# Kernel tuning notes

Measured on AMD Instinct MI355X. Metric: run time of the kernel, lower is better.

Reference implementation:

```python
import jax, jax.numpy as jnp
import numpy as np

N_NODES = 50000
N_EDGES = 600000
N_GRAPHS = 64
D_IN = 128
D_HID = 128
D_OUT = 64


def setup_inputs() -> dict:
    key = jax.random.key(0)
    ks = jax.random.split(key, 8)
    x = jax.random.normal(ks[0], (N_NODES, D_IN), dtype=jnp.float32)
    edge_index = jax.random.randint(ks[1], (2, N_EDGES), 0, N_NODES, dtype=jnp.int64)
    batch = jnp.sort(jax.random.randint(ks[2], (N_NODES,), 0, N_GRAPHS, dtype=jnp.int64))
    def glorot(k, fan_in, fan_out):
        s = jnp.sqrt(6.0 / (fan_in + fan_out))
        return jax.random.uniform(k, (fan_in, fan_out), jnp.float32, -s, s)
    return {
        "x": x, "edge_index": edge_index, "batch": batch,
        "W1": glorot(ks[3], D_IN, D_HID), "b1": jnp.zeros((D_HID,), jnp.float32),
        "W2": glorot(ks[4], D_HID, D_HID), "b2": jnp.zeros((D_HID,), jnp.float32),
        "W3": glorot(ks[5], D_HID, D_HID), "b3": jnp.zeros((D_HID,), jnp.float32),
        "W4": glorot(ks[6], D_HID, D_OUT), "b4": jnp.zeros((D_OUT,), jnp.float32),
    }


def _gcn_conv(x, W, b, src, dst, deg_inv_sqrt, n_nodes):
    # PyG GCNConv: h = x W; out_i = sum_{j->i} norm_ij h_j  (+ self loop) + b
    h = x @ W  # [N, F]
    norm = deg_inv_sqrt[src] * deg_inv_sqrt[dst]  # [E]
    agg = jax.ops.segment_sum(h[src] * norm[:, None], dst, num_segments=n_nodes)
    # self-loop contribution: norm_ii = deg_inv_sqrt[i]^2
    agg = agg + h * (deg_inv_sqrt * deg_inv_sqrt)[:, None]
    return agg + b


def reference(x, edge_index, batch, W1, b1, W2, b2, W3, b3, W4, b4):
    n = x.shape[0]
    src, dst = edge_index[0], edge_index[1]
    # degree including self loops (PyG add_self_loops + deg over dst)
    deg = jax.ops.segment_sum(jnp.ones_like(dst, dtype=x.dtype), dst, num_segments=n) + 1.0
    deg_inv_sqrt = jax.lax.rsqrt(deg)

    h = jax.nn.relu(_gcn_conv(x, W1, b1, src, dst, deg_inv_sqrt, n))
    h = jax.nn.relu(_gcn_conv(h, W2, b2, src, dst, deg_inv_sqrt, n))
    h = jax.nn.relu(_gcn_conv(h, W3, b3, src, dst, deg_inv_sqrt, n))
    h = _gcn_conv(h, W4, b4, src, dst, deg_inv_sqrt, n)

    # global mean pool over graphs in the batch
    sums = jax.ops.segment_sum(h, batch, num_segments=N_GRAPHS)  # [G, D_OUT]
    cnts = jax.ops.segment_sum(jnp.ones((n,), h.dtype), batch, num_segments=N_GRAPHS)
    hg = sums / jnp.maximum(cnts, 1.0)[:, None]
    return jnp.squeeze(hg)
```

## Files before the change

### kernel.cpp

```cpp
#include <hip/hip_runtime.h>
#include <hip/hip_bf16.h>
#include <hip/hip_fp16.h>

#define N_NODES 50000
#define N_EDGES 600000
#define N_GRAPHS 64
#define PCHUNK 16

typedef __attribute__((ext_vector_type(8))) short bf16x8;
typedef __attribute__((ext_vector_type(4))) float f32x4;

__device__ __forceinline__ unsigned short f2bf(float f) {
    unsigned int u = __float_as_uint(f);
    unsigned int r = u + 0x7fffu + ((u >> 16) & 1u);
    return (unsigned short)(r >> 16);
}
__device__ __forceinline__ float bf_lo(unsigned int u) { return __uint_as_float(u << 16); }
__device__ __forceinline__ float bf_hi(unsigned int u) { return __uint_as_float(u & 0xffff0000u); }
__device__ __forceinline__ float bf1(unsigned short s) {
    return __uint_as_float((unsigned int)s << 16);
}
__device__ __forceinline__ float pnorm(unsigned int e) {
    return __half2float(__ushort_as_half((unsigned short)(e & 0xffffu)));
}

__device__ __forceinline__ void wprep_one(const float* W, unsigned short* Wp, int F, int idx) {
    int i = idx & 7;
    int lane = (idx >> 3) & 63;
    int ks = (idx >> 9) & 3;
    int ct = idx >> 11;
    int k = ks * 32 + (lane >> 4) * 8 + i;
    int col = ct * 16 + (lane & 15);
    Wp[idx] = f2bf(W[(size_t)k * F + col]);
}

__global__ __launch_bounds__(256) void deg_wprep(const int* __restrict__ dst,
                                                 int* __restrict__ degi, int E,
                                                 const float* __restrict__ W1,
                                                 const float* __restrict__ W2,
                                                 const float* __restrict__ W3,
                                                 const float* __restrict__ W4,
                                                 unsigned short* __restrict__ Wp1,
                                                 unsigned short* __restrict__ Wp2,
                                                 unsigned short* __restrict__ Wp3,
                                                 unsigned short* __restrict__ Wp4) {
    const int DEGB = (N_EDGES + 255) / 256;
    int bid = blockIdx.x;
    if (bid < DEGB) {
        int i = bid * 256 + threadIdx.x;
        if (i < E) atomicAdd(&degi[dst[i]], 1);
    } else {
        int wb = bid - DEGB;
        if (wb < 64) wprep_one(W1, Wp1, 128, wb * 256 + threadIdx.x);
        else if (wb < 128) wprep_one(W2, Wp2, 128, (wb - 64) * 256 + threadIdx.x);
        else if (wb < 192) wprep_one(W3, Wp3, 128, (wb - 128) * 256 + threadIdx.x);
        else wprep_one(W4, Wp4, 64, (wb - 192) * 256 + threadIdx.x);
    }
}

__global__ __launch_bounds__(256) void scan_block(const int* __restrict__ in,
                                                  int* __restrict__ excl,
                                                  int* __restrict__ bsum,
                                                  float* __restrict__ dis, int N) {
    __shared__ int s[256];
    int i = blockIdx.x * 256 + threadIdx.x;
    int v = (i < N) ? in[i] : 0;
    s[threadIdx.x] = v;
    __syncthreads();
#pragma unroll
    for (int off = 1; off < 256; off <<= 1) {
        int t = (threadIdx.x >= off) ? s[threadIdx.x - off] : 0;
        __syncthreads();
        s[threadIdx.x] += t;
        __syncthreads();
    }
    if (i < N) {
        excl[i] = s[threadIdx.x] - v;
        dis[i] = rsqrtf((float)v + 1.0f);
    }
    if (threadIdx.x == 255) bsum[blockIdx.x] = s[255];
}

__global__ __launch_bounds__(256) void scan_top(const int* __restrict__ bsum,
                                                int* __restrict__ boff, int NB,
                                                const int* __restrict__ batch,
                                                int* __restrict__ gstart, int N) {
    __shared__ int s[256];
    int v = (threadIdx.x < NB) ? bsum[threadIdx.x] : 0;
    s[threadIdx.x] = v;
    __syncthreads();
#pragma unroll
    for (int off = 1; off < 256; off <<= 1) {
        int t = (threadIdx.x >= off) ? s[threadIdx.x - off] : 0;
        __syncthreads();
        s[threadIdx.x] += t;
        __syncthreads();
    }
    if (threadIdx.x < NB) boff[threadIdx.x] = s[threadIdx.x] - v;

    int g = threadIdx.x;
    if (g <= N_GRAPHS) {
        int lo = 0, hi = N;
        while (lo < hi) {
            int mid = (lo + hi) >> 1;
            if (batch[mid] < g) lo = mid + 1; else hi = mid;
        }
        gstart[g] = lo;
    }
}

__global__ __launch_bounds__(256) void scan_fix(const int* __restrict__ excl,
                                                const int* __restrict__ boff,
                                                int* __restrict__ rowptr,
                                                int* __restrict__ cursor, int N, int E) {
    int i = blockIdx.x * 256 + threadIdx.x;
    if (i < N) {
        int r = excl[i] + boff[blockIdx.x];
        rowptr[i] = r;
        cursor[i] = r;
    }
    if (i == 0) rowptr[N] = E;
}

#define MM1B ((N_NODES + 63) / 64)
#define CSRB ((N_EDGES + 255) / 256)

__global__ __launch_bounds__(256) void csrfill_mm1(const int* __restrict__ src,
                                                   const int* __restrict__ dst,
                                                   const float* __restrict__ dis,
                                                   int* __restrict__ cursor,
                                                   unsigned int* __restrict__ csr, int E,
                                                   const float* __restrict__ Xf,
                                                   const unsigned short* __restrict__ Wp,
                                                   unsigned short* __restrict__ T, int N) {
    if (blockIdx.x >= MM1B) {
        const int part = blockIdx.x & 7;
        const int ch = (blockIdx.x - MM1B) >> 3;
        int e = ch * 256 + threadIdx.x;
        if (e >= E) return;
        int d = dst[e];
        if ((d * 8) / N_NODES != part) return;
        int s = src[e];
        float nrm = dis[s] * dis[d];
        unsigned short hb = __half_as_ushort(__float2half(nrm));
        int pos = atomicAdd(&cursor[d], 1);
        csr[pos] = ((unsigned int)s << 16) | (unsigned int)hb;
        return;
    }
    const int lane = threadIdx.x & 63;
    const int wave = threadIdx.x >> 6;
    const int r0 = blockIdx.x * 64 + wave * 16;
    const int kg = lane >> 4;
    const int rdrow = min(r0 + (lane & 15), N - 1);
    const float* xr = Xf + (size_t)rdrow * 128;

    bf16x8 a[4];
#pragma unroll
    for (int ks = 0; ks < 4; ++ks) {
        const int kb = ks * 32 + kg * 8;
        float4 x0 = *reinterpret_cast<const float4*>(xr + kb);
        float4 x1 = *reinterpret_cast<const float4*>(xr + kb + 4);
        float v[8] = {x0.x, x0.y, x0.z, x0.w, x1.x, x1.y, x1.z, x1.w};
#pragma unroll
        for (int i = 0; i < 8; ++i) a[ks][i] = (short)f2bf(v[i]);
    }

#pragma unroll
    for (int ct = 0; ct < 8; ++ct) {
        f32x4 acc = {0.f, 0.f, 0.f, 0.f};
#pragma unroll
        for (int ks = 0; ks < 4; ++ks) {
            bf16x8 b = *reinterpret_cast<const bf16x8*>(Wp + ((size_t)(ct * 4 + ks) * 64 + lane) * 8);
            acc = __builtin_amdgcn_mfma_f32_16x16x32_bf16(a[ks], b, acc, 0, 0, 0);
        }
        const int col = ct * 16 + (lane & 15);
#pragma unroll
        for (int r = 0; r < 4; ++r) {
            const int rowm = r0 + kg * 4 + r;
            if (rowm < N) T[(size_t)rowm * 128 + col] = f2bf(acc[r]);
        }
    }
}

__device__ __forceinline__ void gather128x2(int beg, int mid, int end,
                                            const unsigned int* __restrict__ csr,
                                            const unsigned short* __restrict__ T, int lane,
                                            float& ax0, float& ay0, float& ax1, float& ay1) {
    int p = beg;
    for (; p + 8 <= end; p += 8) {
        unsigned int e0 = csr[p], e1 = csr[p + 1], e2 = csr[p + 2], e3 = csr[p + 3];
        unsigned int e4 = csr[p + 4], e5 = csr[p + 5], e6 = csr[p + 6], e7 = csr[p + 7];
        unsigned int r0 = *reinterpret_cast<const unsigned int*>(T + (size_t)(e0 >> 16) * 128 + lane * 2);
        unsigned int r1 = *reinterpret_cast<const unsigned int*>(T + (size_t)(e1 >> 16) * 128 + lane * 2);
        unsigned int r2 = *reinterpret_cast<const unsigned int*>(T + (size_t)(e2 >> 16) * 128 + lane * 2);
        unsigned int r3 = *reinterpret_cast<const unsigned int*>(T + (size_t)(e3 >> 16) * 128 + lane * 2);
        unsigned int r4 = *reinterpret_cast<const unsigned int*>(T + (size_t)(e4 >> 16) * 128 + lane * 2);
        unsigned int r5 = *reinterpret_cast<const unsigned int*>(T + (size_t)(e5 >> 16) * 128 + lane * 2);
        unsigned int r6 = *reinterpret_cast<const unsigned int*>(T + (size_t)(e6 >> 16) * 128 + lane * 2);
        unsigned int r7 = *reinterpret_cast<const unsigned int*>(T + (size_t)(e7 >> 16) * 128 + lane * 2);
#define ACC8(K)                                                                  \
        {                                                                        \
            float n = pnorm(e##K);                                               \
            float na = (p + K < mid) ? n : 0.0f;                                 \
            float nb = (p + K < mid) ? 0.0f : n;                                 \
            ax0 = fmaf(na, bf_lo(r##K), ax0); ay0 = fmaf(na, bf_hi(r##K), ay0);  \
            ax1 = fmaf(nb, bf_lo(r##K), ax1); ay1 = fmaf(nb, bf_hi(r##K), ay1);  \
        }
        ACC8(0) ACC8(1) ACC8(2) ACC8(3) ACC8(4) ACC8(5) ACC8(6) ACC8(7)
#undef ACC8
    }
    for (; p + 4 <= end; p += 4) {
        unsigned int e0 = csr[p], e1 = csr[p + 1], e2 = csr[p + 2], e3 = csr[p + 3];
        unsigned int r0 = *reinterpret_cast<const unsigned int*>(T + (size_t)(e0 >> 16) * 128 + lane * 2);
        unsigned int r1 = *reinterpret_cast<const unsigned int*>(T + (size_t)(e1 >> 16) * 128 + lane * 2);
        unsigned int r2 = *reinterpret_cast<const unsigned int*>(T + (size_t)(e2 >> 16) * 128 + lane * 2);
        unsigned int r3 = *reinterpret_cast<const unsigned int*>(T + (size_t)(e3 >> 16) * 128 + lane * 2);
#define ACC4(K)                                                                  \
        {                                                                        \
            float n = pnorm(e##K);                                               \
            float na = (p + K < mid) ? n : 0.0f;                                 \
            float nb = (p + K < mid) ? 0.0f : n;                                 \
            ax0 = fmaf(na, bf_lo(r##K), ax0); ay0 = fmaf(na, bf_hi(r##K), ay0);  \
            ax1 = fmaf(nb, bf_lo(r##K), ax1); ay1 = fmaf(nb, bf_hi(r##K), ay1);  \
        }
        ACC4(0) ACC4(1) ACC4(2) ACC4(3)
#undef ACC4
    }
    for (; p < end; ++p) {
        unsigned int e = csr[p];
        unsigned int r = *reinterpret_cast<const unsigned int*>(T + (size_t)(e >> 16) * 128 + lane * 2);
        float n = pnorm(e);
        float na = (p < mid) ? n : 0.0f;
        float nb = (p < mid) ? 0.0f : n;
        ax0 = fmaf(na, bf_lo(r), ax0); ay0 = fmaf(na, bf_hi(r), ay0);
        ax1 = fmaf(nb, bf_lo(r), ax1); ay1 = fmaf(nb, bf_hi(r), ay1);
    }
}

template <int FOUT>
__global__ __launch_bounds__(512) void aggmm(const int* __restrict__ rowptr,
                                             const unsigned int* __restrict__ csr,
                                             const float* __restrict__ dis,
                                             const float* __restrict__ b,
                                             const unsigned short* __restrict__ T,
                                             const unsigned short* __restrict__ Wp,
                                             unsigned short* __restrict__ Tout, int N) {
    __shared__ unsigned short hl[16][136];
    const int lane = threadIdx.x & 63;
    const int wave = threadIdx.x >> 6;
    const int r0 = blockIdx.x * 16;
    const float2 bb = *reinterpret_cast<const float2*>(b + lane * 2);

    const int n0 = __builtin_amdgcn_readfirstlane(r0 + wave * 2);
    const int beg = rowptr[n0];
    const int mid = rowptr[n0 + 1];
    const int end = rowptr[n0 + 2];
    const float d0 = dis[n0], d1 = dis[n0 + 1];

    unsigned int s0 = *reinterpret_cast<const unsigned int*>(T + (size_t)n0 * 128 + lane * 2);
    unsigned int s1 = *reinterpret_cast<const unsigned int*>(T + (size_t)(n0 + 1) * 128 + lane * 2);
    float ax0 = fmaf(bf_lo(s0), d0 * d0, bb.x);
    float ay0 = fmaf(bf_hi(s0), d0 * d0, bb.y);
    float ax1 = fmaf(bf_lo(s1), d1 * d1, bb.x);
    float ay1 = fmaf(bf_hi(s1), d1 * d1, bb.y);

    gather128x2(beg, mid, end, csr, T, lane, ax0, ay0, ax1, ay1);

    *reinterpret_cast<unsigned int*>(&hl[wave * 2 + 0][lane * 2]) =
        ((unsigned int)f2bf(ay0) << 16) | (unsigned int)f2bf(ax0);
    *reinterpret_cast<unsigned int*>(&hl[wave * 2 + 1][lane * 2]) =
        ((unsigned int)f2bf(ay1) << 16) | (unsigned int)f2bf(ax1);
    __syncthreads();

    constexpr int NCT = FOUT / 16;
    if (wave < NCT) {
        const int kg = lane >> 4;
        bf16x8 a[4];
#pragma unroll
        for (int ks = 0; ks < 4; ++ks) {
            bf16x8 av = *reinterpret_cast<const bf16x8*>(&hl[lane & 15][ks * 32 + kg * 8]);
#pragma unroll
            for (int i = 0; i < 8; ++i) av[i] = (av[i] < 0) ? (short)0 : av[i];
            a[ks] = av;
        }

        const int ct = wave;
        f32x4 acc = {0.f, 0.f, 0.f, 0.f};
#pragma unroll
        for (int ks = 0; ks < 4; ++ks) {
            bf16x8 bfr = *reinterpret_cast<const bf16x8*>(Wp + ((size_t)(ct * 4 + ks) * 64 + lane) * 8);
            acc = __builtin_amdgcn_mfma_f32_16x16x32_bf16(a[ks], bfr, acc, 0, 0, 0);
        }
        const int col = ct * 16 + (lane & 15);
#pragma unroll
        for (int r = 0; r < 4; ++r) {
            Tout[(size_t)(r0 + kg * 4 + r) * FOUT + col] = f2bf(acc[r]);
        }
    }
}

__global__ __launch_bounds__(256) void agg64(const int* __restrict__ rowptr,
                                             const unsigned int* __restrict__ csr,
                                             const float* __restrict__ dis,
                                             const float* __restrict__ b,
                                             const unsigned short* __restrict__ T,
                                             unsigned short* __restrict__ H, int N) {
    const int lane = threadIdx.x & 63;
    const int n0 = __builtin_amdgcn_readfirstlane(((blockIdx.x * 256 + threadIdx.x) >> 6) * 2);
    if (n0 >= N) return;

    const int beg = rowptr[n0];
    const int mid = rowptr[n0 + 1];
    const int end = rowptr[n0 + 2];
    const float d0 = dis[n0], d1 = dis[n0 + 1];
    const float blane = b[lane];
    float a0 = fmaf(bf1(T[(size_t)n0 * 64 + lane]), d0 * d0, blane);
    float a1 = fmaf(bf1(T[(size_t)(n0 + 1) * 64 + lane]), d1 * d1, blane);

    int p = beg;
    for (; p + 8 <= end; p += 8) {
        unsigned int e0 = csr[p], e1 = csr[p + 1], e2 = csr[p + 2], e3 = csr[p + 3];
        unsigned int e4 = csr[p + 4], e5 = csr[p + 5], e6 = csr[p + 6], e7 = csr[p + 7];
        unsigned short v0 = T[(size_t)(e0 >> 16) * 64 + lane];
        unsigned short v1 = T[(size_t)(e1 >> 16) * 64 + lane];
        unsigned short v2 = T[(size_t)(e2 >> 16) * 64 + lane];
        unsigned short v3 = T[(size_t)(e3 >> 16) * 64 + lane];
        unsigned short v4 = T[(size_t)(e4 >> 16) * 64 + lane];
        unsigned short v5 = T[(size_t)(e5 >> 16) * 64 + lane];
        unsigned short v6 = T[(size_t)(e6 >> 16) * 64 + lane];
        unsigned short v7 = T[(size_t)(e7 >> 16) * 64 + lane];
#define A64(K)                                                       \
        {                                                            \
            float n = pnorm(e##K);                                   \
            float na = (p + K < mid) ? n : 0.0f;                     \
            float nb = (p + K < mid) ? 0.0f : n;                     \
            a0 = fmaf(na, bf1(v##K), a0);                            \
            a1 = fmaf(nb, bf1(v##K), a1);                            \
        }
        A64(0) A64(1) A64(2) A64(3) A64(4) A64(5) A64(6) A64(7)
#undef A64
    }
    for (; p < end; ++p) {
        unsigned int e = csr[p];
        unsigned short v = T[(size_t)(e >> 16) * 64 + lane];
        float n = pnorm(e);
        float na = (p < mid) ? n : 0.0f;
        float nb = (p < mid) ? 0.0f : n;
        a0 = fmaf(na, bf1(v), a0);
        a1 = fmaf(nb, bf1(v), a1);
    }
    H[(size_t)n0 * 64 + lane] = f2bf(a0);
    H[(size_t)(n0 + 1) * 64 + lane] = f2bf(a1);
}

__global__ __launch_bounds__(256) void pool_partial(const unsigned short* __restrict__ H,
                                                    const int* __restrict__ gstart,
                                                    float* __restrict__ partial) {
    const int g = blockIdx.x >> 4;
    const int c = blockIdx.x & (PCHUNK - 1);
    const int beg = gstart[g], end = gstart[g + 1];
    const int len = end - beg;
    const int csz = (len + PCHUNK - 1) / PCHUNK;
    const int cb = beg + c * csz;
    const int ce = min(cb + csz, end);
    const int lane = threadIdx.x & 63;
    const int wave = threadIdx.x >> 6;

    float acc = 0.0f;
    for (int n = cb + wave; n < ce; n += 4)
        acc += bf1(H[(size_t)n * 64 + lane]);

    __shared__ float s[4][64];
    s[wave][lane] = acc;
    __syncthreads();
    if (wave == 0)
        partial[(size_t)(g * PCHUNK + c) * 64 + lane] =
            s[0][lane] + s[1][lane] + s[2][lane] + s[3][lane];
}

__global__ __launch_bounds__(64) void pool_fin(const float* __restrict__ partial,
                                               const int* __restrict__ gstart,
                                               float* __restrict__ out) {
    const int g = blockIdx.x;
    const int lane = threadIdx.x;
    float v = 0.0f;
#pragma unroll
    for (int c = 0; c < PCHUNK; ++c) v += partial[(size_t)(g * PCHUNK + c) * 64 + lane];
    float cnt = (float)(gstart[g + 1] - gstart[g]);
    out[g * 64 + lane] = v / fmaxf(cnt, 1.0f);
}

extern "C" void kernel_launch(void* const* d_in, const int* in_sizes, int n_in,
                              void* d_out, int out_size, void* d_ws, size_t ws_size,
                              hipStream_t stream) {
    const float* x = (const float*)d_in[0];
    const int* ei = (const int*)d_in[1];
    const int* batch = (const int*)d_in[2];
    const float* W1 = (const float*)d_in[3];
    const float* b1 = (const float*)d_in[4];
    const float* W2 = (const float*)d_in[5];
    const float* b2 = (const float*)d_in[6];
    const float* W3 = (const float*)d_in[7];
    const float* b3 = (const float*)d_in[8];
    const float* W4 = (const float*)d_in[9];
    const float* b4 = (const float*)d_in[10];

    const int N = N_NODES, E = N_EDGES;
    const int* src = ei;
    const int* dst = ei + E;

    char* base = (char*)d_ws;
    size_t off = 0;
    auto carve = [&](size_t bytes) -> void* {
        off = (off + 63) & ~(size_t)63;
        void* p = base + off;
        off += bytes;
        return p;
    };
    unsigned short* Ta = (unsigned short*)carve((size_t)N * 128 * 2);
    unsigned short* Tb = (unsigned short*)carve((size_t)N * 128 * 2);
    unsigned short* H = (unsigned short*)carve((size_t)N * 64 * 2);
    int* degi = (int*)carve((size_t)N * 4);
    float* dis = (float*)carve((size_t)N * 4);
    int* rowptr = (int*)carve((size_t)(N + 1) * 4);
    int* cursor = (int*)carve((size_t)N * 4);
    int* excl = (int*)carve((size_t)N * 4);
    int* bsum = (int*)carve(256 * 4);
    int* boff = (int*)carve(256 * 4);
    unsigned int* csr = (unsigned int*)carve((size_t)E * 4);
    int* gstart = (int*)carve(65 * 4);
    float* partial = (float*)carve((size_t)N_GRAPHS * PCHUNK * 64 * 4);
    unsigned short* Wp1 = (unsigned short*)carve(128 * 128 * 2);
    unsigned short* Wp2 = (unsigned short*)carve(128 * 128 * 2);
    unsigned short* Wp3 = (unsigned short*)carve(128 * 128 * 2);
    unsigned short* Wp4 = (unsigned short*)carve(128 * 64 * 2);

    hipMemsetAsync(degi, 0, N * sizeof(int), stream);

    const int NB = (N + 255) / 256;
    const int DEGB = (E + 255) / 256;
    deg_wprep<<<DEGB + 224, 256, 0, stream>>>(dst, degi, E, W1, W2, W3, W4,
                                              Wp1, Wp2, Wp3, Wp4);
    scan_block<<<NB, 256, 0, stream>>>(degi, excl, bsum, dis, N);
    scan_top<<<1, 256, 0, stream>>>(bsum, boff, NB, batch, gstart, N);
    scan_fix<<<NB, 256, 0, stream>>>(excl, boff, rowptr, cursor, N, E);
    csrfill_mm1<<<MM1B + 8 * CSRB, 256, 0, stream>>>(src, dst, dis, cursor, csr, E,
                                                     x, Wp1, Ta, N);

    const int FUS = (N + 15) / 16;

    aggmm<128><<<FUS, 512, 0, stream>>>(rowptr, csr, dis, b1, Ta, Wp2, Tb, N);
    aggmm<128><<<FUS, 512, 0, stream>>>(rowptr, csr, dis, b2, Tb, Wp3, Ta, N);
    aggmm<64><<<FUS, 512, 0, stream>>>(rowptr, csr, dis, b3, Ta, Wp4, Tb, N);
    agg64<<<(N / 2 * 64 + 255) / 256, 256, 0, stream>>>(rowptr, csr, dis, b4, Tb, H, N);

    pool_partial<<<N_GRAPHS * PCHUNK, 256, 0, stream>>>(H, gstart, partial);
    pool_fin<<<N_GRAPHS, 64, 0, stream>>>(partial, gstart, (float*)d_out);
}
```

Measured before the change: 181.8 us.

## Fuse last-layer aggregation into mean pooling via edge-range summation

The final GCN layer is linear, so its aggregation is folded straight into the per-graph pool. Each pooling block sums the self-loop terms over a node range and the normalized neighbor terms over the graph's contiguous CSR edge range. The bias becomes count*b4, added in the final reduction. This drops the agg64 kernel and the bf16 H intermediate with its write and re-read. The degree histogram also now loads four dst indices per thread with int4. The edge-range split depends on the batch vector being sorted, so that nodes of a graph are contiguous in CSR order.

```diff
diff --git a/kernel.cpp b/kernel.cpp
--- a/kernel.cpp
+++ b/kernel.cpp
@@ -5,7 +5,7 @@
 #define N_NODES 50000
 #define N_EDGES 600000
 #define N_GRAPHS 64
-#define PCHUNK 16
+#define P4C 64
 
 typedef __attribute__((ext_vector_type(8))) short bf16x8;
 typedef __attribute__((ext_vector_type(4))) float f32x4;
@@ -33,6 +33,8 @@
     int col = ct * 16 + (lane & 15);
     Wp[idx] = f2bf(W[(size_t)k * F + col]);
 }
+
+#define DEGB4 ((N_EDGES + 1023) / 1024)
 
 __global__ __launch_bounds__(256) void deg_wprep(const int* __restrict__ dst,
                                                  int* __restrict__ degi, int E,
@@ -44,13 +46,20 @@
                                                  unsigned short* __restrict__ Wp2,
                                                  unsigned short* __restrict__ Wp3,
                                                  unsigned short* __restrict__ Wp4) {
-    const int DEGB = (N_EDGES + 255) / 256;
     int bid = blockIdx.x;
-    if (bid < DEGB) {
-        int i = bid * 256 + threadIdx.x;
-        if (i < E) atomicAdd(&degi[dst[i]], 1);
+    if (bid < DEGB4) {
+        int i4 = bid * 1024 + threadIdx.x * 4;
+        if (i4 + 4 <= E) {
+            int4 d = *reinterpret_cast<const int4*>(dst + i4);
+            atomicAdd(&degi[d.x], 1);
+            atomicAdd(&degi[d.y], 1);
+            atomicAdd(&degi[d.z], 1);
+            atomicAdd(&degi[d.w], 1);
+        } else {
+            for (int i = i4; i < E; ++i) atomicAdd(&degi[dst[i]], 1);
+        }
     } else {
-        int wb = bid - DEGB;
+        int wb = bid - DEGB4;
         if (wb < 64) wprep_one(W1, Wp1, 128, wb * 256 + threadIdx.x);
         else if (wb < 128) wprep_one(W2, Wp2, 128, (wb - 64) * 256 + threadIdx.x);
         else if (wb < 192) wprep_one(W3, Wp3, 128, (wb - 128) * 256 + threadIdx.x);
@@ -299,94 +308,83 @@
     }
 }
 
-__global__ __launch_bounds__(256) void agg64(const int* __restrict__ rowptr,
+__global__ __launch_bounds__(256) void pool4(const int* __restrict__ rowptr,
                                              const unsigned int* __restrict__ csr,
                                              const float* __restrict__ dis,
-                                             const float* __restrict__ b,
                                              const unsigned short* __restrict__ T,
-                                             unsigned short* __restrict__ H, int N) {
-    const int lane = threadIdx.x & 63;
-    const int n0 = __builtin_amdgcn_readfirstlane(((blockIdx.x * 256 + threadIdx.x) >> 6) * 2);
-    if (n0 >= N) return;
-
-    const int beg = rowptr[n0];
-    const int mid = rowptr[n0 + 1];
-    const int end = rowptr[n0 + 2];
-    const float d0 = dis[n0], d1 = dis[n0 + 1];
-    const float blane = b[lane];
-    float a0 = fmaf(bf1(T[(size_t)n0 * 64 + lane]), d0 * d0, blane);
-    float a1 = fmaf(bf1(T[(size_t)(n0 + 1) * 64 + lane]), d1 * d1, blane);
-
-    int p = beg;
-    for (; p + 8 <= end; p += 8) {
-        unsigned int e0 = csr[p], e1 = csr[p + 1], e2 = csr[p + 2], e3 = csr[p + 3];
-        unsigned int e4 = csr[p + 4], e5 = csr[p + 5], e6 = csr[p + 6], e7 = csr[p + 7];
-        unsigned short v0 = T[(size_t)(e0 >> 16) * 64 + lane];
-        unsigned short v1 = T[(size_t)(e1 >> 16) * 64 + lane];
-        unsigned short v2 = T[(size_t)(e2 >> 16) * 64 + lane];
-        unsigned short v3 = T[(size_t)(e3 >> 16) * 64 + lane];
-        unsigned short v4 = T[(size_t)(e4 >> 16) * 64 + lane];
-        unsigned short v5 = T[(size_t)(e5 >> 16) * 64 + lane];
-        unsigned short v6 = T[(size_t)(e6 >> 16) * 64 + lane];
-        unsigned short v7 = T[(size_t)(e7 >> 16) * 64 + lane];
-#define A64(K)                                                       \
-        {                                                            \
-            float n = pnorm(e##K);                                   \
-            float na = (p + K < mid) ? n : 0.0f;                     \
-            float nb = (p + K < mid) ? 0.0f : n;                     \
-            a0 = fmaf(na, bf1(v##K), a0);                            \
-            a1 = fmaf(nb, bf1(v##K), a1);                            \
-        }
-        A64(0) A64(1) A64(2) A64(3) A64(4) A64(5) A64(6) A64(7)
-#undef A64
-    }
-    for (; p < end; ++p) {
-        unsigned int e = csr[p];
-        unsigned short v = T[(size_t)(e >> 16) * 64 + lane];
-        float n = pnorm(e);
-        float na = (p < mid) ? n : 0.0f;
-        float nb = (p < mid) ? 0.0f : n;
-        a0 = fmaf(na, bf1(v), a0);
-        a1 = fmaf(nb, bf1(v), a1);
-    }
-    H[(size_t)n0 * 64 + lane] = f2bf(a0);
-    H[(size_t)(n0 + 1) * 64 + lane] = f2bf(a1);
-}
-
-__global__ __launch_bounds__(256) void pool_partial(const unsigned short* __restrict__ H,
-                                                    const int* __restrict__ gstart,
-                                                    float* __restrict__ partial) {
-    const int g = blockIdx.x >> 4;
-    const int c = blockIdx.x & (PCHUNK - 1);
-    const int beg = gstart[g], end = gstart[g + 1];
-    const int len = end - beg;
-    const int csz = (len + PCHUNK - 1) / PCHUNK;
-    const int cb = beg + c * csz;
-    const int ce = min(cb + csz, end);
+                                             const int* __restrict__ gstart,
+                                             float* __restrict__ partial) {
+    const int g = blockIdx.x / P4C;
+    const int c = blockIdx.x % P4C;
     const int lane = threadIdx.x & 63;
     const int wave = threadIdx.x >> 6;
+    const int nb = gstart[g], ne = gstart[g + 1];
 
     float acc = 0.0f;
-    for (int n = cb + wave; n < ce; n += 4)
-        acc += bf1(H[(size_t)n * 64 + lane]);
+
+    {
+        const int len = ne - nb;
+        const int cs = (len + P4C - 1) / P4C;
+        const int a = nb + c * cs;
+        const int bnd = min(a + cs, ne);
+        for (int n = a + wave; n < bnd; n += 4) {
+            float d = dis[n];
+            acc = fmaf(bf1(T[(size_t)n * 64 + lane]) * d, d, acc);
+        }
+    }
+
+    {
+        const int eb = rowptr[nb], ee = rowptr[ne];
+        const int len = ee - eb;
+        const int cs = (len + P4C - 1) / P4C;
+        const int a = eb + c * cs;
+        const int bnd = min(a + cs, ee);
+        int p = a + wave;
+        for (; p + 8 * 4 <= bnd; p += 32) {
+            unsigned int e0 = csr[p], e1 = csr[p + 4], e2 = csr[p + 8], e3 = csr[p + 12];
+            unsigned int e4 = csr[p + 16], e5 = csr[p + 20], e6 = csr[p + 24], e7 = csr[p + 28];
+            unsigned short v0 = T[(size_t)(e0 >> 16) * 64 + lane];
+            unsigned short v1 = T[(size_t)(e1 >> 16) * 64 + lane];
+            unsigned short v2 = T[(size_t)(e2 >> 16) * 64 + lane];
+            unsigned short v3 = T[(size_t)(e3 >> 16) * 64 + lane];
+            unsigned short v4 = T[(size_t)(e4 >> 16) * 64 + lane];
+            unsigned short v5 = T[(size_t)(e5 >> 16) * 64 + lane];
+            unsigned short v6 = T[(size_t)(e6 >> 16) * 64 + lane];
+            unsigned short v7 = T[(size_t)(e7 >> 16) * 64 + lane];
+            acc = fmaf(pnorm(e0), bf1(v0), acc);
+            acc = fmaf(pnorm(e1), bf1(v1), acc);
+            acc = fmaf(pnorm(e2), bf1(v2), acc);
+            acc = fmaf(pnorm(e3), bf1(v3), acc);
+            acc = fmaf(pnorm(e4), bf1(v4), acc);
+            acc = fmaf(pnorm(e5), bf1(v5), acc);
+            acc = fmaf(pnorm(e6), bf1(v6), acc);
+            acc = fmaf(pnorm(e7), bf1(v7), acc);
+        }
+        for (; p < bnd; p += 4) {
+            unsigned int e = csr[p];
+            acc = fmaf(pnorm(e), bf1(T[(size_t)(e >> 16) * 64 + lane]), acc);
+        }
+    }
 
     __shared__ float s[4][64];
     s[wave][lane] = acc;
     __syncthreads();
     if (wave == 0)
-        partial[(size_t)(g * PCHUNK + c) * 64 + lane] =
+        partial[(size_t)blockIdx.x * 64 + lane] =
             s[0][lane] + s[1][lane] + s[2][lane] + s[3][lane];
 }
 
-__global__ __launch_bounds__(64) void pool_fin(const float* __restrict__ partial,
-                                               const int* __restrict__ gstart,
-                                               float* __restrict__ out) {
+__global__ __launch_bounds__(64) void pool_fin4(const float* __restrict__ partial,
+                                                const int* __restrict__ gstart,
+                                                const float* __restrict__ b4,
+                                                float* __restrict__ out) {
     const int g = blockIdx.x;
     const int lane = threadIdx.x;
     float v = 0.0f;
-#pragma unroll
-    for (int c = 0; c < PCHUNK; ++c) v += partial[(size_t)(g * PCHUNK + c) * 64 + lane];
+#pragma unroll 8
+    for (int c = 0; c < P4C; ++c) v += partial[(size_t)(g * P4C + c) * 64 + lane];
     float cnt = (float)(gstart[g + 1] - gstart[g]);
+    v += cnt * b4[lane];
     out[g * 64 + lane] = v / fmaxf(cnt, 1.0f);
 }
 
@@ -419,7 +417,6 @@
     };
     unsigned short* Ta = (unsigned short*)carve((size_t)N * 128 * 2);
     unsigned short* Tb = (unsigned short*)carve((size_t)N * 128 * 2);
-    unsigned short* H = (unsigned short*)carve((size_t)N * 64 * 2);
     int* degi = (int*)carve((size_t)N * 4);
     float* dis = (float*)carve((size_t)N * 4);
     int* rowptr = (int*)carve((size_t)(N + 1) * 4);
@@ -429,7 +426,7 @@
     int* boff = (int*)carve(256 * 4);
     unsigned int* csr = (unsigned int*)carve((size_t)E * 4);
     int* gstart = (int*)carve(65 * 4);
-    float* partial = (float*)carve((size_t)N_GRAPHS * PCHUNK * 64 * 4);
+    float* partial = (float*)carve((size_t)N_GRAPHS * P4C * 64 * 4);
     unsigned short* Wp1 = (unsigned short*)carve(128 * 128 * 2);
     unsigned short* Wp2 = (unsigned short*)carve(128 * 128 * 2);
     unsigned short* Wp3 = (unsigned short*)carve(128 * 128 * 2);
@@ -438,9 +435,8 @@
     hipMemsetAsync(degi, 0, N * sizeof(int), stream);
 
     const int NB = (N + 255) / 256;
-    const int DEGB = (E + 255) / 256;
-    deg_wprep<<<DEGB + 224, 256, 0, stream>>>(dst, degi, E, W1, W2, W3, W4,
-                                              Wp1, Wp2, Wp3, Wp4);
+    deg_wprep<<<DEGB4 + 224, 256, 0, stream>>>(dst, degi, E, W1, W2, W3, W4,
+                                               Wp1, Wp2, Wp3, Wp4);
     scan_block<<<NB, 256, 0, stream>>>(degi, excl, bsum, dis, N);
     scan_top<<<1, 256, 0, stream>>>(bsum, boff, NB, batch, gstart, N);
     scan_fix<<<NB, 256, 0, stream>>>(excl, boff, rowptr, cursor, N, E);
@@ -452,8 +448,7 @@
     aggmm<128><<<FUS, 512, 0, stream>>>(rowptr, csr, dis, b1, Ta, Wp2, Tb, N);
     aggmm<128><<<FUS, 512, 0, stream>>>(rowptr, csr, dis, b2, Tb, Wp3, Ta, N);
     aggmm<64><<<FUS, 512, 0, stream>>>(rowptr, csr, dis, b3, Ta, Wp4, Tb, N);
-    agg64<<<(N / 2 * 64 + 255) / 256, 256, 0, stream>>>(rowptr, csr, dis, b4, Tb, H, N);
-
-    pool_partial<<<N_GRAPHS * PCHUNK, 256, 0, stream>>>(H, gstart, partial);
-    pool_fin<<<N_GRAPHS, 64, 0, stream>>>(partial, gstart, (float*)d_out);
-}
+
+    pool4<<<N_GRAPHS * P4C, 256, 0, stream>>>(rowptr, csr, dis, Tb, gstart, partial);
+    pool_fin4<<<N_GRAPHS, 64, 0, stream>>>(partial, gstart, b4, (float*)d_out);
+}
```

After: 182.0 us. About the same (+0.2%).
